# Kernel optimization log

Measured on AMD Instinct MI355X. Metric: run time of the kernel, lower is better.

The kernel has to match this reference:

```python
import jax, jax.numpy as jnp
import numpy as np

N = 100000          # nodes
E = 1600000         # edges (avg degree 16)
BAG = 10            # feature ids per node
VOCAB = 50000
D_EMB, D_HID, D_OUT = 128, 64, 32


def setup_inputs() -> dict:
    key = jax.random.key(0)
    ks = jax.random.split(key, 10)
    s = lambda d: 1.0 / np.sqrt(d)
    return {
        "feature_indices": jax.random.randint(ks[0], (N * BAG,), 0, VOCAB),
        "feature_offsets": jnp.arange(N, dtype=jnp.int64) * BAG,
        "edge_index": jax.random.randint(ks[1], (2, E), 0, N),
        "emb_table": jax.random.normal(ks[2], (VOCAB, D_EMB), jnp.float32) * 0.02,
        "W1": jax.random.normal(ks[3], (D_EMB, D_HID), jnp.float32) * s(D_EMB),
        "b1": jnp.zeros((D_HID,), jnp.float32),
        "W_mu": jax.random.normal(ks[4], (D_HID, D_OUT), jnp.float32) * s(D_HID),
        "b_mu": jnp.zeros((D_OUT,), jnp.float32),
        "W_ls": jax.random.normal(ks[5], (D_HID, D_OUT), jnp.float32) * s(D_HID),
        "b_ls": jnp.zeros((D_OUT,), jnp.float32),
        "noise": jax.random.normal(ks[6], (N, D_OUT), jnp.float32),
    }


def _embedding_bag_mean(table, indices, offsets, n_bags):
    # torch.nn.EmbeddingBag(mode='mean') with offsets: bag b spans
    # indices[offsets[b] : offsets[b+1]].
    total = indices.shape[0]
    seg = jnp.searchsorted(offsets, jnp.arange(total), side="right") - 1  # [total]
    emb = table[indices]                                                    # [total, D]
    sums = jax.ops.segment_sum(emb, seg, num_segments=n_bags)               # [N, D]
    counts = jnp.diff(jnp.concatenate([offsets, jnp.array([total], offsets.dtype)]))
    return sums / jnp.maximum(counts, 1)[:, None].astype(sums.dtype)


def _gcn_conv(x, W, b, src, dst, norm, n_nodes):
    # GCNConv: linear -> gather -> normalize -> scatter-add -> bias
    h = x @ W                                   # [N, out]
    msg = h[src] * norm[:, None]                # [E+N, out]
    return jax.ops.segment_sum(msg, dst, num_segments=n_nodes) + b


def reference(feature_indices, feature_offsets, edge_index, emb_table,
              W1, b1, W_mu, b_mu, W_ls, b_ls, noise):
    n = noise.shape[0]
    x = _embedding_bag_mean(emb_table, feature_indices, feature_offsets, n)

    # symmetric GCN normalization with self loops (PyG gcn_norm defaults)
    loop = jnp.arange(n)
    src = jnp.concatenate([edge_index[0], loop])
    dst = jnp.concatenate([edge_index[1], loop])
    deg = jax.ops.segment_sum(jnp.ones_like(src, jnp.float32), dst, num_segments=n)
    dinv = jax.lax.rsqrt(jnp.maximum(deg, 1.0))
    norm = dinv[src] * dinv[dst]                # [E+N]

    h = jax.nn.relu(_gcn_conv(x, W1, b1, src, dst, norm, n))
    mu = _gcn_conv(h, W_mu, b_mu, src, dst, norm, n)
    logstd = _gcn_conv(h, W_ls, b_ls, src, dst, norm, n)
    z = mu + noise * jnp.exp(logstd)            # reparameterize

    # decode: edge-wise dot product + sigmoid on the positive edges
    logits = jnp.sum(z[edge_index[0]] * z[edge_index[1]], axis=1)  # [E]
    return jax.nn.sigmoid(logits)
```

## Files before the change

### kernel.cpp

```cpp
#include <hip/hip_runtime.h>
#include <hip/hip_fp16.h>
#include <math.h>

#define DEMB 128
#define DHID 64
#define DOUT 32
#define BAG  10
#define CAP  64

typedef unsigned int   u32;
typedef unsigned short u16;

__device__ __forceinline__ float bf2f(u16 u) {
    union { u32 i; float f; } c; c.i = (u32)u << 16; return c.f;
}
__device__ __forceinline__ u16 f2bf(float f) {
    union { float f; u32 i; } c; c.f = f;
    u32 r = c.i + 0x7FFFu + ((c.i >> 16) & 1u);
    return (u16)(r >> 16);
}
__device__ __forceinline__ void bf2x(u32 v, float& lo, float& hi) {
    union { u32 i; float f; } a, b;
    a.i = v << 16; b.i = v & 0xFFFF0000u;
    lo = a.f; hi = b.f;
}
__device__ __forceinline__ u32 pack2(float f0, float f1) {
    return (u32)f2bf(f0) | ((u32)f2bf(f1) << 16);
}
__device__ __forceinline__ float2 h2f2(u32 v) {
    __half2 h; *reinterpret_cast<u32*>(&h) = v;
    return __half22float2(h);
}
__device__ __forceinline__ u32 f2h2(float a, float b) {
    __half2 h = __floats2half2_rn(a, b);
    return *reinterpret_cast<u32*>(&h);
}

__global__ __launch_bounds__(256) void fusedA(const int* __restrict__ src,
                                              const int* __restrict__ dst, int E,
                                              int* __restrict__ degc, int* __restrict__ adj,
                                              const float* __restrict__ T,
                                              const float* __restrict__ W1,
                                              u16* __restrict__ TW, int V) {
    const int b = blockIdx.x;
    const int nbb = (E + 255) >> 8;
    const int grp = b / 3, rem = b - grp * 3;
    const bool is_build = (rem == 2) && (grp < nbb);
    if (is_build) {
        int e = grp * 256 + threadIdx.x;
        if (e < E) {
            int d = dst[e];
            int r = atomicAdd(&degc[d], 1);
            if (r < CAP) adj[(size_t)d * CAP + r] = src[e];
        }
        return;
    }
    __shared__ float Ws[DEMB * DHID];
    int before = grp < nbb ? grp : nbb;
    int gb = b - before;
    const int nbg = (V + 3) >> 2;
    if (gb >= nbg) return;
    for (int i = threadIdx.x; i < DEMB * DHID; i += 256) Ws[i] = W1[i];
    __syncthreads();
    int row = gb * 4 + (threadIdx.x >> 6);
    int col = threadIdx.x & 63;
    if (row >= V) return;
    const float* trow = T + (size_t)row * DEMB;
    float acc = 0.f;
#pragma unroll 8
    for (int k = 0; k < DEMB; ++k) acc = fmaf(trow[k], Ws[k * DHID + col], acc);
    TW[(size_t)row * DHID + col] = f2bf(acc);
}

__global__ void emb_bag(const int* __restrict__ idx, const u16* __restrict__ TW,
                        const int* __restrict__ degc, u16* __restrict__ h0, int n) {
    int t = blockIdx.x * blockDim.x + threadIdx.x;
    int node = t >> 3, d8 = t & 7;
    if (node >= n) return;
    const int* bi = idx + (size_t)node * BAG;
    float a[8] = {0.f, 0.f, 0.f, 0.f, 0.f, 0.f, 0.f, 0.f};
#pragma unroll
    for (int j = 0; j < BAG; ++j) {
        uint4 v = *reinterpret_cast<const uint4*>(TW + (size_t)bi[j] * DHID + d8 * 8);
        float f0, f1; bf2x(v.x, f0, f1); a[0] += f0; a[1] += f1;
        bf2x(v.y, f0, f1); a[2] += f0; a[3] += f1;
        bf2x(v.z, f0, f1); a[4] += f0; a[5] += f1;
        bf2x(v.w, f0, f1); a[6] += f0; a[7] += f1;
    }
    float s = rsqrtf((float)(degc[node] + 1)) * (1.0f / (float)BAG);
    uint4 o;
    o.x = pack2(a[0] * s, a[1] * s);
    o.y = pack2(a[2] * s, a[3] * s);
    o.z = pack2(a[4] * s, a[5] * s);
    o.w = pack2(a[6] * s, a[7] * s);
    *reinterpret_cast<uint4*>(h0 + (size_t)node * DHID + d8 * 8) = o;
}

__device__ __forceinline__ void acc_row(const u16* __restrict__ base, float* a) {
    uint4 v = *reinterpret_cast<const uint4*>(base);
    float f0, f1; bf2x(v.x, f0, f1); a[0] += f0; a[1] += f1;
    bf2x(v.y, f0, f1); a[2] += f0; a[3] += f1;
    bf2x(v.z, f0, f1); a[4] += f0; a[5] += f1;
    bf2x(v.w, f0, f1); a[6] += f0; a[7] += f1;
}

#define HPAD 68
__global__ __launch_bounds__(256) void conv1mm(const u16* __restrict__ h0,
                                               const int* __restrict__ degc,
                                               const int* __restrict__ adj,
                                               const float* __restrict__ b1,
                                               const float* __restrict__ Wmu,
                                               const float* __restrict__ Wls,
                                               u16* __restrict__ hcat, int n) {
    __shared__ u16   Wp[DHID * DHID];
    __shared__ float hs[32][HPAD];
    for (int i = threadIdx.x; i < DHID * DHID; i += 256) {
        int k = i >> 6, p = i & 63;
        int j = p >> 3, c = p & 7;
        float w = (c < 4) ? Wmu[k * DOUT + j * 4 + c] : Wls[k * DOUT + j * 4 + (c - 4)];
        Wp[i] = f2bf(w);
    }
    int t = blockIdx.x * 256 + threadIdx.x;
    int node = t >> 3, d8 = t & 7;
    int lnode = threadIdx.x >> 3;
    int dc = 0;
    if (node < n) {
        dc = degc[node];
        int deg = dc < CAP ? dc : CAP;
        const int* ap = adj + (size_t)node * CAP;
        float a[8] = {0.f, 0.f, 0.f, 0.f, 0.f, 0.f, 0.f, 0.f};
        acc_row(h0 + (size_t)node * DHID + d8 * 8, a);
        int k = 0;
        for (; k + 4 <= deg; k += 4) {
            int4 ss = *reinterpret_cast<const int4*>(ap + k);
            acc_row(h0 + (size_t)ss.x * DHID + d8 * 8, a);
            acc_row(h0 + (size_t)ss.y * DHID + d8 * 8, a);
            acc_row(h0 + (size_t)ss.z * DHID + d8 * 8, a);
            acc_row(h0 + (size_t)ss.w * DHID + d8 * 8, a);
        }
        for (; k < deg; ++k) acc_row(h0 + (size_t)ap[k] * DHID + d8 * 8, a);

        float di = rsqrtf((float)(dc + 1));
        float4 b0 = *reinterpret_cast<const float4*>(b1 + d8 * 8);
        float4 b4 = *reinterpret_cast<const float4*>(b1 + d8 * 8 + 4);
        float4 o0, o1;
        o0.x = fmaxf(fmaf(di, a[0], b0.x), 0.f);
        o0.y = fmaxf(fmaf(di, a[1], b0.y), 0.f);
        o0.z = fmaxf(fmaf(di, a[2], b0.z), 0.f);
        o0.w = fmaxf(fmaf(di, a[3], b0.w), 0.f);
        o1.x = fmaxf(fmaf(di, a[4], b4.x), 0.f);
        o1.y = fmaxf(fmaf(di, a[5], b4.y), 0.f);
        o1.z = fmaxf(fmaf(di, a[6], b4.z), 0.f);
        o1.w = fmaxf(fmaf(di, a[7], b4.w), 0.f);
        *reinterpret_cast<float4*>(&hs[lnode][d8 * 8])     = o0;
        *reinterpret_cast<float4*>(&hs[lnode][d8 * 8 + 4]) = o1;
    }
    __syncthreads();
    if (node >= n) return;
    float acc[8] = {0.f, 0.f, 0.f, 0.f, 0.f, 0.f, 0.f, 0.f};
#pragma unroll 4
    for (int k = 0; k < DHID; ++k) {
        float hv = hs[lnode][k];
        uint4 wv = *reinterpret_cast<const uint4*>(&Wp[k * DHID + d8 * 8]);
        float f0, f1;
        bf2x(wv.x, f0, f1); acc[0] = fmaf(hv, f0, acc[0]); acc[1] = fmaf(hv, f1, acc[1]);
        bf2x(wv.y, f0, f1); acc[2] = fmaf(hv, f0, acc[2]); acc[3] = fmaf(hv, f1, acc[3]);
        bf2x(wv.z, f0, f1); acc[4] = fmaf(hv, f0, acc[4]); acc[5] = fmaf(hv, f1, acc[5]);
        bf2x(wv.w, f0, f1); acc[6] = fmaf(hv, f0, acc[6]); acc[7] = fmaf(hv, f1, acc[7]);
    }
    float di = rsqrtf((float)(dc + 1));
    uint4 o;
    o.x = pack2(acc[0] * di, acc[1] * di);
    o.y = pack2(acc[2] * di, acc[3] * di);
    o.z = pack2(acc[4] * di, acc[5] * di);
    o.w = pack2(acc[6] * di, acc[7] * di);
    *reinterpret_cast<uint4*>(hcat + (size_t)node * DHID + d8 * 8) = o;
}

__device__ __forceinline__ void acc_row2i(const u16* __restrict__ row, int j,
                                          float* am, float* al) {
    uint4 v = *reinterpret_cast<const uint4*>(row + j * 8);
    float f0, f1;
    bf2x(v.x, f0, f1); am[0] += f0; am[1] += f1;
    bf2x(v.y, f0, f1); am[2] += f0; am[3] += f1;
    bf2x(v.z, f0, f1); al[0] += f0; al[1] += f1;
    bf2x(v.w, f0, f1); al[2] += f0; al[3] += f1;
}

__global__ void gather_conv2(const u16* __restrict__ hcat, const int* __restrict__ degc,
                             const int* __restrict__ adj,
                             const float* __restrict__ bmu, const float* __restrict__ bls,
                             const float* __restrict__ noise, __half* __restrict__ z, int n) {
    int t = blockIdx.x * blockDim.x + threadIdx.x;
    int node = t >> 3, j = t & 7;
    if (node >= n) return;
    int dc = degc[node];
    int deg = dc < CAP ? dc : CAP;
    const int* ap = adj + (size_t)node * CAP;
    float am[4] = {0.f, 0.f, 0.f, 0.f};
    float al[4] = {0.f, 0.f, 0.f, 0.f};
    acc_row2i(hcat + (size_t)node * DHID, j, am, al);
    int k = 0;
    for (; k + 4 <= deg; k += 4) {
        int4 ss = *reinterpret_cast<const int4*>(ap + k);
        acc_row2i(hcat + (size_t)ss.x * DHID, j, am, al);
        acc_row2i(hcat + (size_t)ss.y * DHID, j, am, al);
        acc_row2i(hcat + (size_t)ss.z * DHID, j, am, al);
        acc_row2i(hcat + (size_t)ss.w * DHID, j, am, al);
    }
    for (; k < deg; ++k) acc_row2i(hcat + (size_t)ap[k] * DHID, j, am, al);

    float di = rsqrtf((float)(dc + 1));
    float4 bm = *reinterpret_cast<const float4*>(bmu + j * 4);
    float4 bl = *reinterpret_cast<const float4*>(bls + j * 4);
    float4 nz = *reinterpret_cast<const float4*>(noise + (size_t)node * DOUT + j * 4);
    float z0 = fmaf(di, am[0], bm.x) + nz.x * expf(fmaf(di, al[0], bl.x));
    float z1 = fmaf(di, am[1], bm.y) + nz.y * expf(fmaf(di, al[1], bl.y));
    float z2 = fmaf(di, am[2], bm.z) + nz.z * expf(fmaf(di, al[2], bl.z));
    float z3 = fmaf(di, am[3], bm.w) + nz.w * expf(fmaf(di, al[3], bl.w));
    uint2 o;
    o.x = f2h2(z0, z1);
    o.y = f2h2(z2, z3);
    *reinterpret_cast<uint2*>(z + (size_t)node * DOUT + j * 4) = o;
}

__global__ void edge_dot(const __half* __restrict__ z, const int* __restrict__ src,
                         const int* __restrict__ dst, float* __restrict__ out, int E) {
    int t = blockIdx.x * blockDim.x + threadIdx.x;
    int e = t >> 2, q = t & 3;
    if (e >= E) return;
    uint4 a = *reinterpret_cast<const uint4*>(z + (size_t)src[e] * DOUT + q * 8);
    uint4 b = *reinterpret_cast<const uint4*>(z + (size_t)dst[e] * DOUT + q * 8);
    float s = 0.f;
    float2 x, y;
    x = h2f2(a.x); y = h2f2(b.x); s += x.x * y.x + x.y * y.y;
    x = h2f2(a.y); y = h2f2(b.y); s += x.x * y.x + x.y * y.y;
    x = h2f2(a.z); y = h2f2(b.z); s += x.x * y.x + x.y * y.y;
    x = h2f2(a.w); y = h2f2(b.w); s += x.x * y.x + x.y * y.y;
    s += __shfl_xor(s, 1);
    s += __shfl_xor(s, 2);
    if (q == 0) out[e] = 1.0f / (1.0f + expf(-s));
}

extern "C" void kernel_launch(void* const* d_in, const int* in_sizes, int n_in,
                              void* d_out, int out_size, void* d_ws, size_t ws_size,
                              hipStream_t stream) {
    const int*   feat_idx = (const int*)d_in[0];
    const int*   edges    = (const int*)d_in[2];
    const float* table    = (const float*)d_in[3];
    const float* W1       = (const float*)d_in[4];
    const float* b1       = (const float*)d_in[5];
    const float* Wmu      = (const float*)d_in[6];
    const float* bmu      = (const float*)d_in[7];
    const float* Wls      = (const float*)d_in[8];
    const float* bls      = (const float*)d_in[9];
    const float* noise    = (const float*)d_in[10];

    const int N = in_sizes[10] / DOUT;
    const int E = in_sizes[2] / 2;
    const int V = in_sizes[3] / DEMB;

    const int* src = edges;
    const int* dst = edges + E;

    char* ws = (char*)d_ws;
    size_t off = 0;
    auto alloc = [&](size_t bytes) { char* p = ws + off; off += (bytes + 255) & ~size_t(255); return p; };
    u16*    tableW = (u16*)   alloc((size_t)V * DHID * 2);
    u16*    h0     = (u16*)   alloc((size_t)N * DHID * 2);
    u16*    hcat   = (u16*)   alloc((size_t)N * DHID * 2);
    __half* zbuf   = (__half*)alloc((size_t)N * DOUT * 2);
    int*    adj    = (int*)   alloc((size_t)N * CAP * 4);
    int*    degc   = (int*)   alloc((size_t)N * 4);
    (void)ws_size;

    hipMemsetAsync(degc, 0, (size_t)N * 4, stream);

    const int B = 256;
    const int nb_build = (E + B - 1) / B;
    const int nb_gemm  = (V + 3) / 4;

    fusedA<<<nb_build + nb_gemm, B, 0, stream>>>(src, dst, E, degc, adj,
                                                 table, W1, tableW, V);

    {
        long long t = (long long)N * 8;
        emb_bag<<<(unsigned)((t + B - 1) / B), B, 0, stream>>>(feat_idx, tableW, degc, h0, N);
    }

    conv1mm<<<(N + 31) / 32, B, 0, stream>>>(h0, degc, adj, b1, Wmu, Wls, hcat, N);

    {
        long long t = (long long)N * 8;
        gather_conv2<<<(unsigned)((t + B - 1) / B), B, 0, stream>>>(hcat, degc, adj,
                                                                    bmu, bls, noise, zbuf, N);
    }

    {
        long long t = (long long)E * 4;
        edge_dot<<<(unsigned)((t + B - 1) / B), B, 0, stream>>>(zbuf, src, dst, (float*)d_out, E);
    }
}
```

Before: 228.8 us.

## Build adjacency via two-pass bucketed binning with LDS-local adjacency assembly

Replaces the per-edge global atomic append into a padded per-node adjacency with a two-pass scheme. The first pass bins edges by 256-node destination bucket into 8 sub-buckets using packed src|local-dst words. A new kernel then assembles each bucket's adjacency and degrees in LDS and writes them out with coalesced vector stores. This is meant to cut scattered global atomics and uncoalesced adjacency writes, at the cost of an extra kernel, a staging buffer, and 64 KB LDS per block. Sub-buckets overflow past 768 edges and source ids are limited to 24 bits.

```diff
diff --git a/kernel.cpp b/kernel.cpp
--- a/kernel.cpp
+++ b/kernel.cpp
@@ -7,6 +7,8 @@
 #define DOUT 32
 #define BAG  10
 #define CAP  64
+#define SUB  8
+#define SUBCAP 768
 
 typedef unsigned int   u32;
 typedef unsigned short u16;
@@ -38,7 +40,7 @@
 
 __global__ __launch_bounds__(256) void fusedA(const int* __restrict__ src,
                                               const int* __restrict__ dst, int E,
-                                              int* __restrict__ degc, int* __restrict__ adj,
+                                              int* __restrict__ cur, u32* __restrict__ bbuf,
                                               const float* __restrict__ T,
                                               const float* __restrict__ W1,
                                               u16* __restrict__ TW, int V) {
@@ -50,8 +52,13 @@
         int e = grp * 256 + threadIdx.x;
         if (e < E) {
             int d = dst[e];
-            int r = atomicAdd(&degc[d], 1);
-            if (r < CAP) adj[(size_t)d * CAP + r] = src[e];
+            int s = src[e];
+            int bkt = d >> 8;
+            int sub = b & 7;
+            int slot = atomicAdd(&cur[bkt * SUB + sub], 1);
+            if (slot < SUBCAP)
+                bbuf[((size_t)bkt * SUB + sub) * SUBCAP + slot] =
+                    (u32)s | ((u32)(d & 255) << 24);
         }
         return;
     }
@@ -70,6 +77,38 @@
 #pragma unroll 8
     for (int k = 0; k < DEMB; ++k) acc = fmaf(trow[k], Ws[k * DHID + col], acc);
     TW[(size_t)row * DHID + col] = f2bf(acc);
+}
+
+__global__ __launch_bounds__(256) void adj_build(const u32* __restrict__ bbuf,
+                                                 const int* __restrict__ cur,
+                                                 int* __restrict__ adj,
+                                                 int* __restrict__ degc,
+                                                 int n, int nbkt) {
+    __shared__ int cnt[256];
+    __shared__ __align__(16) int adjS[256 * CAP];
+    const int b = blockIdx.x;
+    cnt[threadIdx.x] = 0;
+    __syncthreads();
+#pragma unroll
+    for (int x = 0; x < SUB; ++x) {
+        int m = cur[b * SUB + x];
+        if (m > SUBCAP) m = SUBCAP;
+        const u32* p = bbuf + ((size_t)b * SUB + x) * SUBCAP;
+        for (int i = threadIdx.x; i < m; i += 256) {
+            u32 v = p[i];
+            int dl = v >> 24;
+            int r = atomicAdd(&cnt[dl], 1);
+            if (r < CAP) adjS[dl * CAP + r] = (int)(v & 0x00FFFFFFu);
+        }
+    }
+    __syncthreads();
+    const int base = b * 256;
+    int nn = n - base; if (nn > 256) nn = 256;
+    if ((int)threadIdx.x < nn) degc[base + threadIdx.x] = cnt[threadIdx.x];
+    int tot4 = nn * 16;
+    int4* gout = reinterpret_cast<int4*>(adj + (size_t)base * CAP);
+    const int4* lin = reinterpret_cast<const int4*>(adjS);
+    for (int i = threadIdx.x; i < tot4; i += 256) gout[i] = lin[i];
 }
 
 __global__ void emb_bag(const int* __restrict__ idx, const u16* __restrict__ TW,
@@ -259,6 +298,7 @@
     const int N = in_sizes[10] / DOUT;
     const int E = in_sizes[2] / 2;
     const int V = in_sizes[3] / DEMB;
+    const int NBKT = (N + 255) >> 8;
 
     const int* src = edges;
     const int* dst = edges + E;
@@ -271,17 +311,21 @@
     u16*    hcat   = (u16*)   alloc((size_t)N * DHID * 2);
     __half* zbuf   = (__half*)alloc((size_t)N * DOUT * 2);
     int*    adj    = (int*)   alloc((size_t)N * CAP * 4);
-    int*    degc   = (int*)   alloc((size_t)N * 4);
+    int*    degc   = (int*)   alloc((size_t)NBKT * 256 * 4);
+    u32*    bbuf   = (u32*)   alloc((size_t)NBKT * SUB * SUBCAP * 4);
+    int*    cur    = (int*)   alloc((size_t)NBKT * SUB * 4);
     (void)ws_size;
 
-    hipMemsetAsync(degc, 0, (size_t)N * 4, stream);
+    hipMemsetAsync(cur, 0, (size_t)NBKT * SUB * 4, stream);
 
     const int B = 256;
     const int nb_build = (E + B - 1) / B;
     const int nb_gemm  = (V + 3) / 4;
 
-    fusedA<<<nb_build + nb_gemm, B, 0, stream>>>(src, dst, E, degc, adj,
+    fusedA<<<nb_build + nb_gemm, B, 0, stream>>>(src, dst, E, cur, bbuf,
                                                  table, W1, tableW, V);
+
+    adj_build<<<NBKT, B, 0, stream>>>(bbuf, cur, adj, degc, N, NBKT);
 
     {
         long long t = (long long)N * 8;
```

Result: slower. 300.4 us (+31.3%).
